# Performance work log

Measured on AMD Instinct MI355X. Metric: run time of the kernel, lower is better.

The kernel has to match this reference:

```python
import jax, jax.numpy as jnp
import numpy as np

DIM = 1024
HEADS = 16
HEAD_DIM = DIM // HEADS


def setup_inputs() -> dict:
    key = jax.random.key(0)
    ks = jax.random.split(key, 5)
    x = jax.random.normal(ks[0], (4, 2048, DIM), dtype=jnp.float32)
    # torch Linear params: weight [out, in], bias [out]
    qkv_w = jax.random.normal(ks[1], (3 * DIM, DIM), dtype=jnp.float32) * (1.0 / np.sqrt(DIM))
    qkv_b = jax.random.normal(ks[2], (3 * DIM,), dtype=jnp.float32) * 0.01
    out_w = jax.random.normal(ks[3], (DIM, DIM), dtype=jnp.float32) * (1.0 / np.sqrt(DIM))
    out_b = jax.random.normal(ks[4], (DIM,), dtype=jnp.float32) * 0.01
    return {"x": x, "qkv_w": qkv_w, "qkv_b": qkv_b, "out_w": out_w, "out_b": out_b}


def reference(x, qkv_w, qkv_b, out_w, out_b):
    b, s, d = x.shape
    scale = 1.0 / np.sqrt(HEAD_DIM)
    qkv = x @ qkv_w.T + qkv_b                      # [b, s, 3d]
    qkv = qkv.reshape(b, s, 3, HEADS, HEAD_DIM)
    qkv = jnp.transpose(qkv, (2, 0, 3, 1, 4))      # [3, b, h, s, hd]
    q, k, v = qkv[0], qkv[1], qkv[2]
    attn = jnp.einsum('bhqd,bhkd->bhqk', q, k) * scale
    attn = jax.nn.softmax(attn, axis=-1)
    out = jnp.einsum('bhqk,bhkd->bhqd', attn, v)   # [b, h, s, hd]
    out = jnp.transpose(out, (0, 2, 1, 3)).reshape(b, s, d)
    return out @ out_w.T + out_b
```

## Files before the change

kernel.cpp:

```cpp
#include <hip/hip_runtime.h>

namespace {

constexpr int DIMC  = 1024;
constexpr int HEADS = 16;
constexpr int HD    = 64;
constexpr int BATCH = 4;
constexpr int SEQ   = 2048;
constexpr float SC2 = 0.18033688011112042f;

typedef __attribute__((ext_vector_type(8))) short short8;
typedef __attribute__((ext_vector_type(4))) float f32x4;

__device__ __forceinline__ unsigned short f2bf(float f) {
    union { float f; unsigned u; } v; v.f = f;
    unsigned r = v.u + 0x7fffu + ((v.u >> 16) & 1u);
    return (unsigned short)(r >> 16);
}

__device__ __forceinline__ void gl16(const unsigned short* gsrc, const unsigned short* ldst) {
    __builtin_amdgcn_global_load_lds(
        (const __attribute__((address_space(1))) void*)gsrc,
        (__attribute__((address_space(3))) void*)ldst, 16, 0, 0);
}

__global__ __launch_bounds__(256) void cvt_f32_bf16(
    const float* __restrict__ in, unsigned short* __restrict__ out, int n8)
{
    for (int i = blockIdx.x * blockDim.x + threadIdx.x; i < n8;
         i += gridDim.x * blockDim.x) {
        const float4 a = ((const float4*)in)[2*i];
        const float4 b = ((const float4*)in)[2*i + 1];
        union { unsigned short s[8]; uint4 u; } p;
        p.s[0]=f2bf(a.x); p.s[1]=f2bf(a.y); p.s[2]=f2bf(a.z); p.s[3]=f2bf(a.w);
        p.s[4]=f2bf(b.x); p.s[5]=f2bf(b.y); p.s[6]=f2bf(b.z); p.s[7]=f2bf(b.w);
        ((uint4*)out)[i] = p.u;
    }
}

template<int OUT_BF16>
__global__ __launch_bounds__(256) void gemm_bf16_mfma(
    const unsigned short* __restrict__ A, const unsigned short* __restrict__ W,
    const float* __restrict__ bias, void* __restrict__ Cout,
    int M, int N, int K)
{
    __shared__ __align__(16) char lds[32768];
    unsigned short* base = (unsigned short*)lds;

    const int tid = threadIdx.x;
    const int w = tid >> 6, l = tid & 63;
    const int wr = w >> 1, wc = w & 1;
    const int fr = l & 15, fq = l >> 4;
    const int row0 = blockIdx.y * 128, col0 = blockIdx.x * 128;

    const int sr0 = (w*2 + 0)*16 + (l >> 2);
    const int sr1 = (w*2 + 1)*16 + (l >> 2);
    const int skz = (((l & 3) ^ ((l >> 3) & 3))) * 8;

    const unsigned short* Ab0 = A + (size_t)(row0 + sr0)*K + skz;
    const unsigned short* Ab1 = A + (size_t)(row0 + sr1)*K + skz;
    const unsigned short* Wb0 = W + (size_t)(col0 + sr0)*K + skz;
    const unsigned short* Wb1 = W + (size_t)(col0 + sr1)*K + skz;

    f32x4 acc[4][4];
#pragma unroll
    for (int mi = 0; mi < 4; ++mi)
#pragma unroll
        for (int ni = 0; ni < 4; ++ni)
#pragma unroll
            for (int r = 0; r < 4; ++r) acc[mi][ni][r] = 0.f;

    const int cfa = (fq ^ ((fr >> 1) & 3)) * 8;

    auto stage = [&](int k0, int buf) {
        unsigned short* Ad = base + buf*8192;
        unsigned short* Wd = Ad + 4096;
        gl16(Ab0 + k0, Ad + (w*2 + 0)*512);
        gl16(Ab1 + k0, Ad + (w*2 + 1)*512);
        gl16(Wb0 + k0, Wd + (w*2 + 0)*512);
        gl16(Wb1 + k0, Wd + (w*2 + 1)*512);
    };

    stage(0, 0);
    for (int k0 = 0; k0 < K; k0 += 32) {
        const int buf = (k0 >> 5) & 1;
        __syncthreads();
        if (k0 + 32 < K) stage(k0 + 32, buf ^ 1);

        const unsigned short* Ac = base + buf*8192;
        const unsigned short* Wc = Ac + 4096;
        short8 af[4], bf[4];
#pragma unroll
        for (int mi = 0; mi < 4; ++mi)
            af[mi] = *(const short8*)(Ac + (wr*64 + mi*16 + fr)*32 + cfa);
#pragma unroll
        for (int ni = 0; ni < 4; ++ni)
            bf[ni] = *(const short8*)(Wc + (wc*64 + ni*16 + fr)*32 + cfa);
#pragma unroll
        for (int mi = 0; mi < 4; ++mi)
#pragma unroll
            for (int ni = 0; ni < 4; ++ni)
                acc[mi][ni] = __builtin_amdgcn_mfma_f32_16x16x32_bf16(
                    af[mi], bf[ni], acc[mi][ni], 0, 0, 0);
    }

    float bv[4];
#pragma unroll
    for (int ni = 0; ni < 4; ++ni) bv[ni] = bias[col0 + wc*64 + ni*16 + fr];
#pragma unroll
    for (int mi = 0; mi < 4; ++mi)
#pragma unroll
        for (int ni = 0; ni < 4; ++ni)
#pragma unroll
            for (int r = 0; r < 4; ++r) acc[mi][ni][r] += bv[ni];

    __syncthreads();
    float* rp = (float*)lds + w*1088;
    const int orow = l >> 2, oc = (l & 3) * 16;
#pragma unroll
    for (int mi = 0; mi < 4; ++mi) {
#pragma unroll
        for (int ni = 0; ni < 4; ++ni)
#pragma unroll
            for (int r = 0; r < 4; ++r)
                rp[(fq*4 + r)*68 + ni*16 + fr] = acc[mi][ni][r];
        float vrow[16];
#pragma unroll
        for (int j = 0; j < 4; ++j)
            *(f32x4*)&vrow[j*4] = *(const f32x4*)&rp[orow*68 + oc + j*4];
        const size_t grow = (size_t)(row0 + wr*64 + mi*16 + orow);
        const int    gcol = col0 + wc*64 + oc;
        if (OUT_BF16) {
            union { unsigned short s[16]; uint4 u[2]; } pk;
#pragma unroll
            for (int j = 0; j < 16; ++j) pk.s[j] = f2bf(vrow[j]);
            uint4* dst = (uint4*)((unsigned short*)Cout + grow*N + gcol);
            dst[0] = pk.u[0]; dst[1] = pk.u[1];
        } else {
            float* dst = (float*)Cout + grow*N + gcol;
#pragma unroll
            for (int j = 0; j < 4; ++j)
                *(f32x4*)(dst + j*4) = *(const f32x4*)&vrow[j*4];
        }
    }
}

__global__ __launch_bounds__(256) void transpose_v(
    const unsigned short* __restrict__ qkvb, unsigned short* __restrict__ vt)
{
    __shared__ __align__(16) unsigned short T[64*72];
    const int tid = threadIdx.x;
    const int s0 = blockIdx.x * 64, h = blockIdx.y, b = blockIdx.z;
    const unsigned short* src = qkvb + (size_t)b*SEQ*3072 + 2048 + h*64;

    const int r = tid >> 2, c0 = (tid & 3) * 16;
    uint4 u0 = *(const uint4*)(src + (size_t)(s0 + r)*3072 + c0);
    uint4 u1 = *(const uint4*)(src + (size_t)(s0 + r)*3072 + c0 + 8);
    unsigned short e[16];
    *(uint4*)&e[0] = u0; *(uint4*)&e[8] = u1;
#pragma unroll
    for (int i = 0; i < 16; ++i) T[(c0 + i)*72 + r] = e[i];
    __syncthreads();
    const int d = tid >> 2, ss = (tid & 3) * 16;
    uint4 w0 = *(const uint4*)(&T[d*72 + ss]);
    uint4 w1 = *(const uint4*)(&T[d*72 + ss + 8]);
    unsigned short* dst = vt + ((size_t)((b*16 + h)*64 + d))*SEQ + s0 + ss;
    *(uint4*)dst = w0; *(uint4*)(dst + 8) = w1;
}

__global__ __launch_bounds__(256) void attn_mfma(
    const unsigned short* __restrict__ qkvb,
    const unsigned short* __restrict__ vt,
    unsigned short* __restrict__ ctxb)
{
    __shared__ __align__(16) char pool[51200];
    unsigned short* Kb0 = (unsigned short*)pool;
    unsigned short* Vb0 = Kb0 + 8192;
    unsigned short* Pl  = Kb0 + 16384;

    const int tid = threadIdx.x, w = tid >> 6, l = tid & 63;
    const int fr = l & 15, fq = l >> 4;

    const int bid = blockIdx.x;
    const int nid = (bid & 7) * 128 + (bid >> 3);
    const int b  = nid >> 8;
    const int h  = (nid >> 4) & 15;
    const int q0 = (nid & 15) * 128;
    const int wq = q0 + w*32;

    const unsigned short* qb = qkvb + (size_t)b*SEQ*3072 + h*64;
    const unsigned short* kb = qb + 1024;
    const unsigned short* vb = vt + (size_t)((b*16 + h)*64)*SEQ;

    auto scale8 = [](short8 v) -> short8 {
        union { short8 s; unsigned u[4]; } in, out;
        in.s = v;
#pragma unroll
        for (int i = 0; i < 4; ++i) {
            const float lo = __uint_as_float(in.u[i] << 16) * SC2;
            const float hi = __uint_as_float(in.u[i] & 0xffff0000u) * SC2;
            unsigned r;
            asm("v_cvt_pk_bf16_f32 %0, %1, %2" : "=v"(r) : "v"(lo), "v"(hi));
            out.u[i] = r;
        }
        return out.s;
    };
    short8 qf[2][2];
#pragma unroll
    for (int mf = 0; mf < 2; ++mf)
#pragma unroll
        for (int kk = 0; kk < 2; ++kk)
            qf[mf][kk] = scale8(*(const short8*)(qb + (size_t)(wq + mf*16 + fr)*3072
                                                 + kk*32 + fq*8));

    short8 ones;
#pragma unroll
    for (int i = 0; i < 8; ++i) ones[i] = (short)0x3F80;

    f32x4 o[2][4];
    f32x4 ol[2];
#pragma unroll
    for (int mf = 0; mf < 2; ++mf) {
#pragma unroll
        for (int df = 0; df < 4; ++df)
#pragma unroll
            for (int r = 0; r < 4; ++r) o[mf][df][r] = 0.f;
#pragma unroll
        for (int r = 0; r < 4; ++r) ol[mf][r] = 0.f;
    }

    const int srA = (w*2 + 0)*8 + (l >> 3);
    const int srB = (w*2 + 1)*8 + (l >> 3);
    const int scz = ((l & 7) ^ (l >> 3)) * 8;
    unsigned short* Pw = Pl + w*2304;

    const int c0e = (fq ^ (fr & 7)) * 8;
    const int c1e = c0e ^ 32;

    auto stage = [&](int kv0, int buf) {
        unsigned short* Kd = Kb0 + buf*4096;
        unsigned short* Vd = Vb0 + buf*4096;
        gl16(kb + (size_t)(kv0 + srA)*3072 + scz, Kd + (w*2 + 0)*512);
        gl16(kb + (size_t)(kv0 + srB)*3072 + scz, Kd + (w*2 + 1)*512);
        gl16(vb + (size_t)srA*SEQ + kv0 + scz,    Vd + (w*2 + 0)*512);
        gl16(vb + (size_t)srB*SEQ + kv0 + scz,    Vd + (w*2 + 1)*512);
    };

    stage(0, 0);
    for (int kv0 = 0; kv0 < SEQ; kv0 += 64) {
        const int buf = (kv0 >> 6) & 1;
        __syncthreads();
        if (kv0 + 64 < SEQ) stage(kv0 + 64, buf ^ 1);

        const unsigned short* Kc = Kb0 + buf*4096;
        const unsigned short* Vc = Vb0 + buf*4096;

        f32x4 s[2][4];
#pragma unroll
        for (int mf = 0; mf < 2; ++mf)
#pragma unroll
            for (int nf = 0; nf < 4; ++nf)
#pragma unroll
                for (int r = 0; r < 4; ++r) s[mf][nf][r] = 0.f;
#pragma unroll
        for (int nf = 0; nf < 4; ++nf) {
            const short8 k0f = *(const short8*)(Kc + (nf*16 + fr)*64 + c0e);
            const short8 k1f = *(const short8*)(Kc + (nf*16 + fr)*64 + c1e);
#pragma unroll
            for (int mf = 0; mf < 2; ++mf) {
                s[mf][nf] = __builtin_amdgcn_mfma_f32_16x16x32_bf16(k0f, qf[mf][0], s[mf][nf], 0,0,0);
                s[mf][nf] = __builtin_amdgcn_mfma_f32_16x16x32_bf16(k1f, qf[mf][1], s[mf][nf], 0,0,0);
            }
        }

#pragma unroll
        for (int mf = 0; mf < 2; ++mf)
#pragma unroll
            for (int nf = 0; nf < 4; ++nf) {
                const float p0 = exp2f(s[mf][nf][0]);
                const float p1 = exp2f(s[mf][nf][1]);
                const float p2 = exp2f(s[mf][nf][2]);
                const float p3 = exp2f(s[mf][nf][3]);
                unsigned u0, u1;
                asm("v_cvt_pk_bf16_f32 %0, %1, %2" : "=v"(u0) : "v"(p0), "v"(p1));
                asm("v_cvt_pk_bf16_f32 %0, %1, %2" : "=v"(u1) : "v"(p2), "v"(p3));
                *(unsigned long long*)(Pw + (mf*16 + fr)*72 + nf*16 + fq*4) =
                    (unsigned long long)u0 | ((unsigned long long)u1 << 32);
            }

        short8 pa[2][2];
#pragma unroll
        for (int mf = 0; mf < 2; ++mf)
#pragma unroll
            for (int kk = 0; kk < 2; ++kk)
                pa[mf][kk] = *(const short8*)(Pw + (mf*16 + fr)*72 + kk*32 + fq*8);
#pragma unroll
        for (int df = 0; df < 4; ++df) {
            const short8 v0f = *(const short8*)(Vc + (df*16 + fr)*64 + c0e);
            const short8 v1f = *(const short8*)(Vc + (df*16 + fr)*64 + c1e);
#pragma unroll
            for (int mf = 0; mf < 2; ++mf) {
                o[mf][df] = __builtin_amdgcn_mfma_f32_16x16x32_bf16(v0f, pa[mf][0], o[mf][df], 0,0,0);
                o[mf][df] = __builtin_amdgcn_mfma_f32_16x16x32_bf16(v1f, pa[mf][1], o[mf][df], 0,0,0);
            }
        }
#pragma unroll
        for (int mf = 0; mf < 2; ++mf) {
            ol[mf] = __builtin_amdgcn_mfma_f32_16x16x32_bf16(ones, pa[mf][0], ol[mf], 0,0,0);
            ol[mf] = __builtin_amdgcn_mfma_f32_16x16x32_bf16(ones, pa[mf][1], ol[mf], 0,0,0);
        }
    }

    __syncthreads();
    float* rp = (float*)(pool + w*8704);
    const float inv0 = 1.f / ol[0][0], inv1 = 1.f / ol[1][0];
#pragma unroll
    for (int df = 0; df < 4; ++df) {
        f32x4 v0 = o[0][df] * inv0;
        f32x4 v1 = o[1][df] * inv1;
        *(f32x4*)&rp[(fr)*68      + df*16 + fq*4] = v0;
        *(f32x4*)&rp[(16 + fr)*68 + df*16 + fq*4] = v1;
    }
    const int orow = l >> 1, oc = (l & 1)*32;
    float vr[32];
#pragma unroll
    for (int j = 0; j < 8; ++j)
        *(f32x4*)&vr[j*4] = *(const f32x4*)&rp[orow*68 + oc + j*4];
    union { unsigned short s[32]; uint4 u[4]; } pk;
#pragma unroll
    for (int j = 0; j < 32; ++j) pk.s[j] = f2bf(vr[j]);
    unsigned short* dst = ctxb + (size_t)(b*SEQ + q0 + w*32 + orow)*DIMC + h*64 + oc;
#pragma unroll
    for (int j = 0; j < 4; ++j) *((uint4*)dst + j) = pk.u[j];
}

}

extern "C" void kernel_launch(void* const* d_in, const int* in_sizes, int n_in,
                              void* d_out, int out_size, void* d_ws, size_t ws_size,
                              hipStream_t stream)
{
    const float* x     = (const float*)d_in[0];
    const float* qkv_w = (const float*)d_in[1];
    const float* qkv_b = (const float*)d_in[2];
    const float* out_w = (const float*)d_in[3];
    const float* out_b = (const float*)d_in[4];

    unsigned short* xb   = (unsigned short*)d_ws;
    unsigned short* wqb  = xb   + (size_t)8192*1024;
    unsigned short* wob  = wqb  + (size_t)3072*1024;
    unsigned short* qkvb = wob  + (size_t)1024*1024;
    unsigned short* vtw  = qkvb + (size_t)8192*3072;
    unsigned short* ctxb = vtw  + (size_t)4096*2048;

    cvt_f32_bf16<<<2048, 256, 0, stream>>>(x,     xb,  8192*1024/8);
    cvt_f32_bf16<<<1024, 256, 0, stream>>>(qkv_w, wqb, 3072*1024/8);
    cvt_f32_bf16<<<512,  256, 0, stream>>>(out_w, wob, 1024*1024/8);

    gemm_bf16_mfma<1><<<dim3(24, 64), 256, 0, stream>>>(
        xb, wqb, qkv_b, (void*)qkvb, 8192, 3072, 1024);

    transpose_v<<<dim3(SEQ/64, HEADS, BATCH), 256, 0, stream>>>(qkvb, vtw);

    attn_mfma<<<dim3(1024), 256, 0, stream>>>(qkvb, vtw, ctxb);

    gemm_bf16_mfma<0><<<dim3(8, 64), 256, 0, stream>>>(
        ctxb, wob, out_b, d_out, 8192, 1024, 1024);
}
```

Measured before the change: 227.1 us.

## Fuse conversion kernels and hoist V fragment loads in attention loop

The three f32-to-bf16 conversion launches become a single grid-stride kernel that picks the source and destination by index range, removing two launches. In the attention inner loop, the V fragments are loaded from LDS before the QK^T MFMAs so their latency can overlap compute. The first QK MFMA now takes a zero accumulator instead of explicitly zeroing the score registers, and the row-sum MFMAs are moved ahead of the PV MFMAs. Holding the V fragments for longer adds register pressure, which could lower occupancy.

```diff
diff --git a/kernel.cpp b/kernel.cpp
--- a/kernel.cpp
+++ b/kernel.cpp
@@ -24,17 +24,27 @@
         (__attribute__((address_space(3))) void*)ldst, 16, 0, 0);
 }
 
-__global__ __launch_bounds__(256) void cvt_f32_bf16(
-    const float* __restrict__ in, unsigned short* __restrict__ out, int n8)
-{
-    for (int i = blockIdx.x * blockDim.x + threadIdx.x; i < n8;
+__global__ __launch_bounds__(256) void cvt3_f32_bf16(
+    const float* __restrict__ x,  const float* __restrict__ wq,
+    const float* __restrict__ wo,
+    unsigned short* __restrict__ xb, unsigned short* __restrict__ wqb,
+    unsigned short* __restrict__ wob)
+{
+    constexpr int N0 = 8192*1024/8;
+    constexpr int N1 = 3072*1024/8;
+    constexpr int N2 = 1024*1024/8;
+    for (int i = blockIdx.x * blockDim.x + threadIdx.x; i < N0 + N1 + N2;
          i += gridDim.x * blockDim.x) {
-        const float4 a = ((const float4*)in)[2*i];
-        const float4 b = ((const float4*)in)[2*i + 1];
+        const float* src; unsigned short* dst; int j;
+        if (i < N0)           { src = x;  dst = xb;  j = i; }
+        else if (i < N0 + N1) { src = wq; dst = wqb; j = i - N0; }
+        else                  { src = wo; dst = wob; j = i - N0 - N1; }
+        const float4 a = ((const float4*)src)[2*j];
+        const float4 b = ((const float4*)src)[2*j + 1];
         union { unsigned short s[8]; uint4 u; } p;
         p.s[0]=f2bf(a.x); p.s[1]=f2bf(a.y); p.s[2]=f2bf(a.z); p.s[3]=f2bf(a.w);
         p.s[4]=f2bf(b.x); p.s[5]=f2bf(b.y); p.s[6]=f2bf(b.z); p.s[7]=f2bf(b.w);
-        ((uint4*)out)[i] = p.u;
+        ((uint4*)dst)[j] = p.u;
     }
 }
 
@@ -217,6 +227,10 @@
 #pragma unroll
     for (int i = 0; i < 8; ++i) ones[i] = (short)0x3F80;
 
+    f32x4 z4;
+#pragma unroll
+    for (int r = 0; r < 4; ++r) z4[r] = 0.f;
+
     f32x4 o[2][4];
     f32x4 ol[2];
 #pragma unroll
@@ -255,20 +269,21 @@
         const unsigned short* Kc = Kb0 + buf*4096;
         const unsigned short* Vc = Vb0 + buf*4096;
 
+        short8 vf[4][2];
+#pragma unroll
+        for (int df = 0; df < 4; ++df) {
+            vf[df][0] = *(const short8*)(Vc + (df*16 + fr)*64 + c0e);
+            vf[df][1] = *(const short8*)(Vc + (df*16 + fr)*64 + c1e);
+        }
+
         f32x4 s[2][4];
-#pragma unroll
-        for (int mf = 0; mf < 2; ++mf)
-#pragma unroll
-            for (int nf = 0; nf < 4; ++nf)
-#pragma unroll
-                for (int r = 0; r < 4; ++r) s[mf][nf][r] = 0.f;
 #pragma unroll
         for (int nf = 0; nf < 4; ++nf) {
             const short8 k0f = *(const short8*)(Kc + (nf*16 + fr)*64 + c0e);
             const short8 k1f = *(const short8*)(Kc + (nf*16 + fr)*64 + c1e);
 #pragma unroll
             for (int mf = 0; mf < 2; ++mf) {
-                s[mf][nf] = __builtin_amdgcn_mfma_f32_16x16x32_bf16(k0f, qf[mf][0], s[mf][nf], 0,0,0);
+                s[mf][nf] = __builtin_amdgcn_mfma_f32_16x16x32_bf16(k0f, qf[mf][0], z4, 0,0,0);
                 s[mf][nf] = __builtin_amdgcn_mfma_f32_16x16x32_bf16(k1f, qf[mf][1], s[mf][nf], 0,0,0);
             }
         }
@@ -284,8 +299,8 @@
                 unsigned u0, u1;
                 asm("v_cvt_pk_bf16_f32 %0, %1, %2" : "=v"(u0) : "v"(p0), "v"(p1));
                 asm("v_cvt_pk_bf16_f32 %0, %1, %2" : "=v"(u1) : "v"(p2), "v"(p3));
-                *(unsigned long long*)(Pw + (mf*16 + fr)*72 + nf*16 + fq*4) =
-                    (unsigned long long)u0 | ((unsigned long long)u1 << 32);
+                uint2 pw; pw.x = u0; pw.y = u1;
+                *(uint2*)(Pw + (mf*16 + fr)*72 + nf*16 + fq*4) = pw;
             }
 
         short8 pa[2][2];
@@ -294,21 +309,18 @@
 #pragma unroll
             for (int kk = 0; kk < 2; ++kk)
                 pa[mf][kk] = *(const short8*)(Pw + (mf*16 + fr)*72 + kk*32 + fq*8);
-#pragma unroll
-        for (int df = 0; df < 4; ++df) {
-            const short8 v0f = *(const short8*)(Vc + (df*16 + fr)*64 + c0e);
-            const short8 v1f = *(const short8*)(Vc + (df*16 + fr)*64 + c1e);
-#pragma unroll
-            for (int mf = 0; mf < 2; ++mf) {
-                o[mf][df] = __builtin_amdgcn_mfma_f32_16x16x32_bf16(v0f, pa[mf][0], o[mf][df], 0,0,0);
-                o[mf][df] = __builtin_amdgcn_mfma_f32_16x16x32_bf16(v1f, pa[mf][1], o[mf][df], 0,0,0);
-            }
-        }
 #pragma unroll
         for (int mf = 0; mf < 2; ++mf) {
             ol[mf] = __builtin_amdgcn_mfma_f32_16x16x32_bf16(ones, pa[mf][0], ol[mf], 0,0,0);
             ol[mf] = __builtin_amdgcn_mfma_f32_16x16x32_bf16(ones, pa[mf][1], ol[mf], 0,0,0);
         }
+#pragma unroll
+        for (int df = 0; df < 4; ++df)
+#pragma unroll
+            for (int mf = 0; mf < 2; ++mf) {
+                o[mf][df] = __builtin_amdgcn_mfma_f32_16x16x32_bf16(vf[df][0], pa[mf][0], o[mf][df], 0,0,0);
+                o[mf][df] = __builtin_amdgcn_mfma_f32_16x16x32_bf16(vf[df][1], pa[mf][1], o[mf][df], 0,0,0);
+            }
     }
 
     __syncthreads();
@@ -353,9 +365,7 @@
     unsigned short* vtw  = qkvb + (size_t)8192*3072;
     unsigned short* ctxb = vtw  + (size_t)4096*2048;
 
-    cvt_f32_bf16<<<2048, 256, 0, stream>>>(x,     xb,  8192*1024/8);
-    cvt_f32_bf16<<<1024, 256, 0, stream>>>(qkv_w, wqb, 3072*1024/8);
-    cvt_f32_bf16<<<512,  256, 0, stream>>>(out_w, wob, 1024*1024/8);
+    cvt3_f32_bf16<<<2048, 256, 0, stream>>>(x, qkv_w, out_w, xb, wqb, wob);
 
     gemm_bf16_mfma<1><<<dim3(24, 64), 256, 0, stream>>>(
         xb, wqb, qkv_b, (void*)qkvb, 8192, 3072, 1024);
```

Result: no change. 224.6 us (-1.1%).
